# Performance work log

Measured on AMD Instinct MI355X. Metric: run time of the kernel, lower is better.

The kernel has to match this reference:

```python
import jax, jax.numpy as jnp
import numpy as np

B, S, D = 1024, 256, 128  # batch, seq_len, emb_dim; concat feat = 4*D = 512
H1, H2 = 256, 64          # att_hidden_size tail; att_hidden_size = [4*D, H1, H2]


def setup_inputs() -> dict:
    key = jax.random.key(0)
    ks = jax.random.split(key, 8)
    queries = jax.random.normal(ks[0], (B, D), dtype=jnp.float32)
    keys = jax.random.normal(ks[1], (B, S, D), dtype=jnp.float32)
    keys_length = jax.random.randint(ks[2], (B,), 1, S + 1)  # in [1, S]
    W1 = jax.random.normal(ks[3], (4 * D, H1), dtype=jnp.float32) * (1.0 / np.sqrt(4 * D))
    b1 = jnp.zeros((H1,), dtype=jnp.float32)
    W2 = jax.random.normal(ks[4], (H1, H2), dtype=jnp.float32) * (1.0 / np.sqrt(H1))
    b2 = jnp.zeros((H2,), dtype=jnp.float32)
    Wd = jax.random.normal(ks[5], (H2, 1), dtype=jnp.float32) * (1.0 / np.sqrt(H2))
    bd = jnp.zeros((1,), dtype=jnp.float32)
    return {"queries": queries, "keys": keys, "keys_length": keys_length,
            "W1": W1, "b1": b1, "W2": W2, "b2": b2, "Wd": Wd, "bd": bd}


def reference(queries, keys, keys_length, W1, b1, W2, b2, Wd, bd):
    # broadcast query across sequence: [B, S, D]
    q = jnp.broadcast_to(queries[:, None, :], keys.shape)
    feat = jnp.concatenate([q, keys, q - keys, q * keys], axis=-1)
    # att MLP (sigmoid after each layer, as in MLPLayers)
    h = jax.nn.sigmoid(jnp.einsum('bsf,fh->bsh', feat, W1) + b1)
    h = jax.nn.sigmoid(jnp.einsum('bsh,hk->bsk', h, W2) + b2)
    score = (jnp.einsum('bsk,ko->bso', h, Wd) + bd)[..., 0]  # [B, S]
    # mask: positions >= keys_length are invalid (mask_mat = arange(S))
    mask = jnp.arange(S)[None, :] >= keys_length[:, None]
    score = jnp.where(mask, -jnp.inf, score)  # softmax_stag=True -> -inf fill
    score = score / jnp.sqrt(jnp.float32(D))
    w = jax.nn.softmax(score, axis=1)  # [B, S]
    # return_seq_weight=False -> weighted sum over keys: [B, 1, D]
    out = jnp.einsum('bs,bsd->bd', w, keys)[:, None, :]
    return out
```

## Files before the change

### kernel.cpp

```cpp
#include <hip/hip_runtime.h>


typedef unsigned short u16;
typedef unsigned int u32;
typedef short bf16x8 __attribute__((ext_vector_type(8)));
typedef float f32x4 __attribute__((ext_vector_type(4)));

#define NBATCH 1024
#define SLEN 256
#define DD 128
#define NH1 256
#define NH2 64

#define WS_WBCT  0
#define WS_WDT   65536
#define WS_W2T   131072
#define WS_WDS   163840
#define WS_WSUM  165888
#define WS_BIAS1 296960

#define L_KBUF   0
#define L_H1     16384
#define L_SCORES 32768
#define L_BIAS   33792
#define L_B2     34816
#define L_WD     35072
#define L_WPART  35344
#define L_RED4   35856
#define L_SIZE   35904

__device__ __forceinline__ u16 f2bf_rne(float f){
  union { float f; unsigned u; } v; v.f = f;
  unsigned r = v.u + 0x7fffu + ((v.u >> 16) & 1u);
  return (u16)(r >> 16);
}
__device__ __forceinline__ u32 pack_trunc(float a, float b){
  return (__float_as_uint(a) >> 16) | (__float_as_uint(b) & 0xffff0000u);
}
__device__ __forceinline__ float b2fl(short s){
  return __uint_as_float(((u32)(u16)s) << 16);
}
__device__ __forceinline__ int swz(int byte){
  return byte ^ (((byte >> 9) & 7) << 4);
}
__device__ __forceinline__ int swzk(int byte){
  return byte ^ (((byte >> 8) & 7) << 4);
}
__device__ __forceinline__ float fsigmoid(float x){
  return __builtin_amdgcn_rcpf(1.f + __expf(-x));
}
__device__ __forceinline__ void barrier_lds(){
  asm volatile("s_waitcnt lgkmcnt(0)" ::: "memory");
  __builtin_amdgcn_s_barrier();
  __builtin_amdgcn_sched_barrier(0);
}

__global__ void prep_weights(const float* __restrict__ W1, const float* __restrict__ W2,
                             const float* __restrict__ Wd, const float* __restrict__ bd,
                             u16* __restrict__ WbcT, u16* __restrict__ WdT,
                             u16* __restrict__ W2T, float* __restrict__ WdS,
                             float* __restrict__ Wsum){
  int n = blockIdx.x;
  int k = threadIdx.x;
  if (k < DD){
    WbcT[n * DD + k] = f2bf_rne(W1[(128 + k) * NH1 + n] - W1[(256 + k) * NH1 + n]);
    WdT [n * DD + k] = f2bf_rne(W1[(384 + k) * NH1 + n]);
    Wsum[k * NH1 + n] = W1[k * NH1 + n] + W1[(256 + k) * NH1 + n];
  }
  if (n < NH2) W2T[n * 256 + k] = f2bf_rne(W2[k * NH2 + n]);
  if (n == 0 && k < NH2) WdS[k] = Wd[k];
  if (n == 0 && k == NH2) WdS[NH2] = bd[0];
}

__global__ void prep_bias(const float* __restrict__ q, const float* __restrict__ Wsum,
                          const float* __restrict__ b1, float* __restrict__ bias1){
  __shared__ float qsh[DD];
  int b = blockIdx.x, j = threadIdx.x;
  if (j < DD) qsh[j] = q[b * DD + j];
  __syncthreads();
  float acc = b1[j];
  #pragma unroll 8
  for (int d = 0; d < DD; ++d)
    acc += qsh[d] * Wsum[d * NH1 + j];
  bias1[b * NH1 + j] = acc;
}

__global__ __launch_bounds__(256, 2)
void seqatt_main(const float* __restrict__ queries, const float* __restrict__ keys,
                 const int* __restrict__ keys_length,
                 const u16* __restrict__ WbcT, const u16* __restrict__ WdT,
                 const u16* __restrict__ W2Tg,
                 const float* __restrict__ WdS, const float* __restrict__ bias1g,
                 const float* __restrict__ b2g, float* __restrict__ out)
{
  __shared__ alignas(16) char smem[L_SIZE];
  float* scores = (float*)(smem + L_SCORES);
  float* bias1s = (float*)(smem + L_BIAS);
  float* b2s    = (float*)(smem + L_B2);
  float* wds    = (float*)(smem + L_WD);
  float* wpart  = (float*)(smem + L_WPART);
  float* red4   = (float*)(smem + L_RED4);

  const int b = blockIdx.x;
  const int tid = threadIdx.x;
  const int lane = tid & 63;
  const int wave = tid >> 6;
  const int l15 = lane & 15;
  const int g   = lane >> 4;
  const int r = tid >> 3, seg = tid & 7;

  bias1s[tid] = bias1g[b * NH1 + tid];
  if (tid < 64) b2s[tid] = b2g[tid];
  if (tid < 65) wds[tid] = WdS[tid];
  const int klen = keys_length[b];
  const float* kbb = keys + (long)b * SLEN * DD;

  float4 k0, k1, k2, k3;
#define ISSUE(t) do { const float* p_ = kbb + (((t) << 5) + r) * DD + (seg << 4); \
    k0 = *(const float4*)p_;       k1 = *(const float4*)(p_ + 4); \
    k2 = *(const float4*)(p_ + 8); k3 = *(const float4*)(p_ + 12); } while (0)
#define STORE(t) do { int bb_ = (((t) & 1) << 13) + (r << 8) + (seg << 5); \
    uint4 w_; \
    w_.x = pack_trunc(k0.x, k0.y); w_.y = pack_trunc(k0.z, k0.w); \
    w_.z = pack_trunc(k1.x, k1.y); w_.w = pack_trunc(k1.z, k1.w); \
    *(uint4*)(smem + swzk(bb_)) = w_; \
    w_.x = pack_trunc(k2.x, k2.y); w_.y = pack_trunc(k2.z, k2.w); \
    w_.z = pack_trunc(k3.x, k3.y); w_.w = pack_trunc(k3.z, k3.w); \
    *(uint4*)(smem + swzk(bb_ + 16)) = w_; } while (0)

  ISSUE(0);

  bf16x8 bfrag[4][4];
  {
    const float* qb = queries + b * DD;
    #pragma unroll
    for (int nt = 0; nt < 4; ++nt){
      int n = (wave << 6) + (nt << 4) + l15;
      #pragma unroll
      for (int kk = 0; kk < 4; ++kk){
        int k0i = (g << 3) + (kk << 5);
        bf16x8 bc = *(const bf16x8*)(WbcT + n * DD + k0i);
        bf16x8 wd = *(const bf16x8*)(WdT  + n * DD + k0i);
        float4 q0 = *(const float4*)(qb + k0i);
        float4 q1 = *(const float4*)(qb + k0i + 4);
        float qa[8] = {q0.x, q0.y, q0.z, q0.w, q1.x, q1.y, q1.z, q1.w};
        union { u16 s[8]; bf16x8 v; } o;
        #pragma unroll
        for (int j = 0; j < 8; ++j)
          o.s[j] = f2bf_rne(fmaf(qa[j], b2fl(wd[j]), b2fl(bc[j])));
        bfrag[nt][kk] = o.v;
      }
    }
  }
  bf16x8 w2frag[8];
  #pragma unroll
  for (int kk = 0; kk < 8; ++kk)
    w2frag[kk] = *(const bf16x8*)(W2Tg + ((wave << 4) + l15) * 256 + (kk << 5) + (g << 3));

  STORE(0);
  barrier_lds();

  const f32x4 fz = {0.f, 0.f, 0.f, 0.f};

  for (int st = 0; st < 8; ++st){
    const int s0 = st << 5;
    const int kb_base = (st & 1) << 13;

    if (st < 7) ISSUE(st + 1);

    f32x4 acc[2][4];
    #pragma unroll
    for (int mt = 0; mt < 2; ++mt)
      #pragma unroll
      for (int nt = 0; nt < 4; ++nt) acc[mt][nt] = fz;
    #pragma unroll
    for (int kk = 0; kk < 4; ++kk){
      bf16x8 af[2];
      #pragma unroll
      for (int mt = 0; mt < 2; ++mt)
        af[mt] = *(const bf16x8*)(smem + swzk(kb_base + (((mt << 4) + l15) << 8) + (kk << 6) + (g << 4)));
      #pragma unroll
      for (int mt = 0; mt < 2; ++mt)
        #pragma unroll
        for (int nt = 0; nt < 4; ++nt)
          acc[mt][nt] = __builtin_amdgcn_mfma_f32_16x16x32_bf16(bfrag[nt][kk], af[mt], acc[mt][nt], 0, 0, 0);
    }

    #pragma unroll
    for (int nt = 0; nt < 4; ++nt){
      float4 bia = *(const float4*)(bias1s + (wave << 6) + (nt << 4) + (g << 2));
      #pragma unroll
      for (int mt = 0; mt < 2; ++mt){
        float v0 = fsigmoid(acc[mt][nt][0] + bia.x);
        float v1 = fsigmoid(acc[mt][nt][1] + bia.y);
        float v2 = fsigmoid(acc[mt][nt][2] + bia.z);
        float v3 = fsigmoid(acc[mt][nt][3] + bia.w);
        uint2 p; p.x = pack_trunc(v0, v1); p.y = pack_trunc(v2, v3);
        int s = (mt << 4) + l15;
        int hb = (wave << 6) + (nt << 4) + (g << 2);
        *(uint2*)(smem + swz(L_H1 + (s << 9) + (hb << 1))) = p;
      }
    }
    barrier_lds();

    f32x4 acc2[2];
    acc2[0] = fz; acc2[1] = fz;
    #pragma unroll
    for (int kk = 0; kk < 8; ++kk){
      bf16x8 a2[2];
      #pragma unroll
      for (int mt = 0; mt < 2; ++mt)
        a2[mt] = *(const bf16x8*)(smem + swz(L_H1 + (((mt << 4) + l15) << 9) + (kk << 6) + (g << 4)));
      #pragma unroll
      for (int mt = 0; mt < 2; ++mt)
        acc2[mt] = __builtin_amdgcn_mfma_f32_16x16x32_bf16(w2frag[kk], a2[mt], acc2[mt], 0, 0, 0);
    }

    {
      float pp0 = 0.f, pp1 = 0.f;
      #pragma unroll
      for (int i = 0; i < 4; ++i){
        int o = (wave << 4) + (g << 2) + i;
        float b2v = b2s[o], wdv = wds[o];
        pp0 += fsigmoid(acc2[0][i] + b2v) * wdv;
        pp1 += fsigmoid(acc2[1][i] + b2v) * wdv;
      }
      pp0 += __shfl_xor(pp0, 16); pp0 += __shfl_xor(pp0, 32);
      pp1 += __shfl_xor(pp1, 16); pp1 += __shfl_xor(pp1, 32);
      if (lane < 16){
        wpart[(wave << 5) + lane]      = pp0;
        wpart[(wave << 5) + 16 + lane] = pp1;
      }
    }

    if (st < 7) STORE(st + 1);

    barrier_lds();

    if (tid < 32){
      float v = wpart[tid] + wpart[32 + tid] + wpart[64 + tid] + wpart[96 + tid];
      int s = s0 + tid;
      scores[s] = (s < klen) ? (v + wds[64]) * 0.08838834764831845f : -1e30f;
    }
  }

  barrier_lds();

  {
    float v = scores[tid];
    float m = v;
    #pragma unroll
    for (int off = 32; off >= 1; off >>= 1) m = fmaxf(m, __shfl_xor(m, off));
    if (lane == 0) red4[wave] = m;
    __syncthreads();
    float mx = fmaxf(fmaxf(red4[0], red4[1]), fmaxf(red4[2], red4[3]));
    float e = __expf(v - mx);
    float ssum = e;
    #pragma unroll
    for (int off = 32; off >= 1; off >>= 1) ssum += __shfl_xor(ssum, off);
    if (lane == 0) red4[4 + wave] = ssum;
    __syncthreads();
    float tot = red4[4] + red4[5] + red4[6] + red4[7];
    scores[tid] = e * __builtin_amdgcn_rcpf(tot);
    __syncthreads();
  }

  {
    float* red = (float*)smem;
    int d = tid & 127, half = tid >> 7;
    const float* kb = keys + ((long)b * SLEN + half * 128) * DD + d;
    float acc = 0.f;
    #pragma unroll 4
    for (int s2 = 0; s2 < 128; ++s2) acc += scores[half * 128 + s2] * kb[s2 * DD];
    red[tid] = acc;
    __syncthreads();
    if (tid < 128) out[b * DD + tid] = red[tid] + red[128 + tid];
  }
#undef ISSUE
#undef STORE
}

extern "C" void kernel_launch(void* const* d_in, const int* in_sizes, int n_in,
                              void* d_out, int out_size, void* d_ws, size_t ws_size,
                              hipStream_t stream) {
  const float* queries     = (const float*)d_in[0];
  const float* keys        = (const float*)d_in[1];
  const int*   keys_length = (const int*)d_in[2];
  const float* W1 = (const float*)d_in[3];
  const float* b1 = (const float*)d_in[4];
  const float* W2 = (const float*)d_in[5];
  const float* b2 = (const float*)d_in[6];
  const float* Wd = (const float*)d_in[7];
  const float* bd = (const float*)d_in[8];
  float* out = (float*)d_out;
  char* ws = (char*)d_ws;

  u16*   WbcT  = (u16*)(ws + WS_WBCT);
  u16*   WdT   = (u16*)(ws + WS_WDT);
  u16*   W2T   = (u16*)(ws + WS_W2T);
  float* WdS   = (float*)(ws + WS_WDS);
  float* Wsum  = (float*)(ws + WS_WSUM);
  float* bias1 = (float*)(ws + WS_BIAS1);

  prep_weights<<<dim3(256), dim3(256), 0, stream>>>(W1, W2, Wd, bd, WbcT, WdT, W2T, WdS, Wsum);
  prep_bias<<<dim3(NBATCH), dim3(256), 0, stream>>>(queries, Wsum, b1, bias1);
  seqatt_main<<<dim3(NBATCH), dim3(256), 0, stream>>>(queries, keys, keys_length,
                                                      WbcT, WdT, W2T, WdS, bias1, b2, out);
}
```

Baseline: 90.23 us.

## Software-pipeline GEMM1 and GEMM2 across sequence tiles with double-buffered H1

Restructures the per-tile loop so GEMM1 for tile t+1 runs in the same phase as GEMM2 for tile t. H1 and the partial-score buffers are double-buffered in LDS, which removes one barrier per tile. Global key loads are issued two tiles ahead. The cost is more LDS use, which can lower occupancy, and register pressure from keeping loads two stages in flight.

Measured after the change: 90.03 us. Within noise of the previous version (-0.2%).

```diff
diff --git a/kernel.cpp b/kernel.cpp
--- a/kernel.cpp
+++ b/kernel.cpp
@@ -21,13 +21,13 @@
 
 #define L_KBUF   0
 #define L_H1     16384
-#define L_SCORES 32768
-#define L_BIAS   33792
-#define L_B2     34816
-#define L_WD     35072
-#define L_WPART  35344
-#define L_RED4   35856
-#define L_SIZE   35904
+#define L_SCORES 49152
+#define L_BIAS   50176
+#define L_B2     51200
+#define L_WD     51456
+#define L_WPART  51728
+#define L_RED4   52752
+#define L_SIZE   52800
 
 __device__ __forceinline__ u16 f2bf_rne(float f){
   union { float f; unsigned u; } v; v.f = f;
@@ -157,17 +157,11 @@
   for (int kk = 0; kk < 8; ++kk)
     w2frag[kk] = *(const bf16x8*)(W2Tg + ((wave << 4) + l15) * 256 + (kk << 5) + (g << 3));
 
-  STORE(0);
-  barrier_lds();
-
   const f32x4 fz = {0.f, 0.f, 0.f, 0.f};
 
-  for (int st = 0; st < 8; ++st){
-    const int s0 = st << 5;
-    const int kb_base = (st & 1) << 13;
-
-    if (st < 7) ISSUE(st + 1);
-
+  auto do_gemm1 = [&](int t){
+    const int kb_base = (t & 1) << 13;
+    const int h_base  = L_H1 + ((t & 1) << 14);
     f32x4 acc[2][4];
     #pragma unroll
     for (int mt = 0; mt < 2; ++mt)
@@ -185,7 +179,6 @@
         for (int nt = 0; nt < 4; ++nt)
           acc[mt][nt] = __builtin_amdgcn_mfma_f32_16x16x32_bf16(bfrag[nt][kk], af[mt], acc[mt][nt], 0, 0, 0);
     }
-
     #pragma unroll
     for (int nt = 0; nt < 4; ++nt){
       float4 bia = *(const float4*)(bias1s + (wave << 6) + (nt << 4) + (g << 2));
@@ -198,11 +191,13 @@
         uint2 p; p.x = pack_trunc(v0, v1); p.y = pack_trunc(v2, v3);
         int s = (mt << 4) + l15;
         int hb = (wave << 6) + (nt << 4) + (g << 2);
-        *(uint2*)(smem + swz(L_H1 + (s << 9) + (hb << 1))) = p;
+        *(uint2*)(smem + swz(h_base + (s << 9) + (hb << 1))) = p;
       }
     }
-    barrier_lds();
-
+  };
+
+  auto do_gemm2 = [&](int t){
+    const int h_base = L_H1 + ((t & 1) << 14);
     f32x4 acc2[2];
     acc2[0] = fz; acc2[1] = fz;
     #pragma unroll
@@ -210,40 +205,56 @@
       bf16x8 a2[2];
       #pragma unroll
       for (int mt = 0; mt < 2; ++mt)
-        a2[mt] = *(const bf16x8*)(smem + swz(L_H1 + (((mt << 4) + l15) << 9) + (kk << 6) + (g << 4)));
+        a2[mt] = *(const bf16x8*)(smem + swz(h_base + (((mt << 4) + l15) << 9) + (kk << 6) + (g << 4)));
       #pragma unroll
       for (int mt = 0; mt < 2; ++mt)
         acc2[mt] = __builtin_amdgcn_mfma_f32_16x16x32_bf16(w2frag[kk], a2[mt], acc2[mt], 0, 0, 0);
     }
-
-    {
-      float pp0 = 0.f, pp1 = 0.f;
-      #pragma unroll
-      for (int i = 0; i < 4; ++i){
-        int o = (wave << 4) + (g << 2) + i;
-        float b2v = b2s[o], wdv = wds[o];
-        pp0 += fsigmoid(acc2[0][i] + b2v) * wdv;
-        pp1 += fsigmoid(acc2[1][i] + b2v) * wdv;
-      }
-      pp0 += __shfl_xor(pp0, 16); pp0 += __shfl_xor(pp0, 32);
-      pp1 += __shfl_xor(pp1, 16); pp1 += __shfl_xor(pp1, 32);
-      if (lane < 16){
-        wpart[(wave << 5) + lane]      = pp0;
-        wpart[(wave << 5) + 16 + lane] = pp1;
-      }
-    }
-
-    if (st < 7) STORE(st + 1);
-
+    float pp0 = 0.f, pp1 = 0.f;
+    #pragma unroll
+    for (int i = 0; i < 4; ++i){
+      int o = (wave << 4) + (g << 2) + i;
+      float b2v = b2s[o], wdv = wds[o];
+      pp0 += fsigmoid(acc2[0][i] + b2v) * wdv;
+      pp1 += fsigmoid(acc2[1][i] + b2v) * wdv;
+    }
+    pp0 += __shfl_xor(pp0, 16); pp0 += __shfl_xor(pp0, 32);
+    pp1 += __shfl_xor(pp1, 16); pp1 += __shfl_xor(pp1, 32);
+    float* wp = wpart + ((t & 1) << 7);
+    if (lane < 16){
+      wp[(wave << 5) + lane]      = pp0;
+      wp[(wave << 5) + 16 + lane] = pp1;
+    }
+  };
+
+  auto finalize = [&](int t){
+    if (tid < 32){
+      const float* wp = wpart + ((t & 1) << 7);
+      float v = wp[tid] + wp[32 + tid] + wp[64 + tid] + wp[96 + tid];
+      int s = (t << 5) + tid;
+      scores[s] = (s < klen) ? (v + wds[64]) * 0.08838834764831845f : -1e30f;
+    }
+  };
+
+  STORE(0);
+  ISSUE(1);
+  barrier_lds();
+  do_gemm1(0);
+  STORE(1);
+  ISSUE(2);
+  barrier_lds();
+
+  for (int t = 0; t < 8; ++t){
+    if (t > 0) finalize(t - 1);
+    if (t < 7) do_gemm1(t + 1);
+    do_gemm2(t);
+    if (t < 6){
+      STORE(t + 2);
+      if (t < 5) ISSUE(t + 3);
+    }
     barrier_lds();
-
-    if (tid < 32){
-      float v = wpart[tid] + wpart[32 + tid] + wpart[64 + tid] + wpart[96 + tid];
-      int s = s0 + tid;
-      scores[s] = (s < klen) ? (v + wds[64]) * 0.08838834764831845f : -1e30f;
-    }
-  }
-
+  }
+  finalize(7);
   barrier_lds();
 
   {
```
